# Kernel tuning notes

Measured on AMD Instinct MI355X. Metric: run time of the kernel, lower is better.

The kernel has to match this reference:

```python
import jax, jax.numpy as jnp
import numpy as np

NUM_HEADS = 16


def setup_inputs() -> dict:
    key = jax.random.key(0)
    ks = jax.random.split(key, 7)
    T, B, E = 2048, 2, 1024
    return {
        "query": jax.random.normal(ks[0], (T, B, E), jnp.float32),
        "key": jax.random.normal(ks[1], (T, B, E), jnp.float32),
        "value": jax.random.normal(ks[2], (T, B, E), jnp.float32),
        "query_pos": jax.random.normal(ks[3], (T, B, E), jnp.float32),
        "key_pos": jax.random.normal(ks[4], (T, B, E), jnp.float32),
        "W": jax.random.normal(ks[5], (E, E), jnp.float32) * (1.0 / np.sqrt(E)),
        "b": jax.random.normal(ks[6], (E,), jnp.float32) * 0.01,
    }


def reference(query, key, value, query_pos, key_pos, W, b):
    T, B, E = query.shape
    S = key.shape[0]
    H = NUM_HEADS
    D = E // H
    scale = jnp.asarray(D ** 0.5, query.dtype)

    identity = query  # residual uses query BEFORE positional add
    q = query + query_pos
    k = key + key_pos

    # (T,B,E) -> (B,H,T,D)
    q = q.reshape(T, B, H, D).transpose(1, 2, 0, 3)
    k = k.reshape(S, B, H, D).transpose(1, 2, 0, 3)
    v = value.reshape(S, B, H, D).transpose(1, 2, 0, 3)

    attn = jnp.einsum("bhtd,bhsd->bhts", q, k) / scale
    attn = jax.nn.softmax(attn, axis=-1)  # dropout p=0 -> identity

    out = jnp.einsum("bhts,bhsd->bhtd", attn, v)
    out = out.transpose(2, 0, 1, 3).reshape(T, B, E)  # (B,H,T,D)->(T,B,E)
    out = out @ W.T + b  # fuse_heads linear; out_dropout p=0 -> identity
    out = out + identity

    attn_avg = attn.sum(axis=1) / H  # average over heads -> (B,T,S)
    return out, attn_avg
```

## Files before the change

### kernel.cpp

```cpp
#include <hip/hip_runtime.h>
#include <hip/hip_bf16.h>

#define T_DIM 2048
#define S_DIM 2048
#define B_DIM 2
#define E_DIM 1024
#define H_DIM 16
#define D_DIM 64
#define EXP2S 0.18033688f
#define EXP2(x) __builtin_amdgcn_exp2f(x)

typedef unsigned short u16;
typedef unsigned int u32;
typedef float v4f __attribute__((ext_vector_type(4)));
typedef short v8s __attribute__((ext_vector_type(8)));
typedef short v4s __attribute__((ext_vector_type(4)));

__device__ __forceinline__ u16 f2bf(float f) {
    union { float f; u32 u; } x; x.f = f;
    return (u16)((x.u + 0x7fffu + ((x.u >> 16) & 1u)) >> 16);
}
__device__ __forceinline__ u32 pkrn(float lo, float hi) {
    union { __hip_bfloat162 h; u32 u; } c;
    c.h = __float22bfloat162_rn(make_float2(lo, hi));
    return c.u;
}
__device__ __forceinline__ v4f mfma16(v8s a, v8s b, v4f c) {
    return __builtin_amdgcn_mfma_f32_16x16x32_bf16(a, b, c, 0, 0, 0);
}
__device__ __forceinline__ v4f mfma16x16(v4s a, v4s b, v4f c) {
    return __builtin_amdgcn_mfma_f32_16x16x16bf16_1k(a, b, c, 0, 0, 0);
}
__device__ __forceinline__ v8s ld8(const u16* p) {
    return *reinterpret_cast<const v8s*>(p);
}

__global__ __launch_bounds__(256) void prep_qk(
    const float* __restrict__ q, const float* __restrict__ qp,
    const float* __restrict__ k, const float* __restrict__ kp,
    u16* __restrict__ qb, u16* __restrict__ ks) {
    int o = blockIdx.x * 256 + threadIdx.x;
    int d = o & 63, t = (o >> 6) & 2047, h = (o >> 17) & 15, b = o >> 21;
    int src = ((t * B_DIM + b) << 10) + (h << 6) + d;
    qb[o] = f2bf((q[src] + qp[src]) * EXP2S);
    ks[o] = f2bf(k[src] + kp[src]);
}

__global__ __launch_bounds__(256) void prep_w(const float* __restrict__ W, u16* __restrict__ Wb) {
    int o = blockIdx.x * 256 + threadIdx.x;
    Wb[o] = f2bf(W[o]);
}

__global__ __launch_bounds__(256) void prep_vt(const float* __restrict__ V, u16* __restrict__ vt) {
    __shared__ float tile[64 * 65];
    int bx = blockIdx.x;
    int bh = bx >> 5;
    int s0 = (bx & 31) * 64;
    int b = bh >> 4, h = bh & 15;
    int tid = threadIdx.x;
    int quarter = tid >> 6, c = tid & 63;
    int boff = b * E_DIM + h * 64;
#pragma unroll
    for (int p = 0; p < 16; ++p) {
        int r = quarter * 16 + p;
        tile[r * 65 + c] = V[(size_t)(s0 + r) * (B_DIM * E_DIM) + boff + c];
    }
    __syncthreads();
#pragma unroll
    for (int p = 0; p < 16; ++p) {
        int d = quarter * 16 + p;
        vt[(size_t)bh * (D_DIM * S_DIM) + (size_t)d * S_DIM + s0 + c] = f2bf(tile[c * 65 + d]);
    }
}

#define PITCH 72
__global__ __launch_bounds__(256) void attn_pv(
    const u16* __restrict__ qb, const u16* __restrict__ ks, const u16* __restrict__ vt,
    float* __restrict__ lin, u16* __restrict__ Xb) {
    __shared__ u16 Kl[2][64 * PITCH];
    __shared__ u16 Vl[2][64 * PITCH];

    int bx = blockIdx.x;
    int bh = bx >> 4;
    int b = bh >> 4, h = bh & 15;
    int tid = threadIdx.x;
    int w = tid >> 6;
    int tbase = (bx & 15) * 128 + w * 32;
    int lane = tid & 63;
    int m = lane & 15, g = lane >> 4;

    int srow = tid >> 2;
    int sqtr = (tid & 3) * 16;

    uint4 kr0, kr1, vr0, vr1;
    auto load_stage = [&](int s0) {
        const uint4* kp = reinterpret_cast<const uint4*>(
            ks + ((size_t)bh * S_DIM + s0 + srow) * 64 + sqtr);
        kr0 = kp[0]; kr1 = kp[1];
        const uint4* vp = reinterpret_cast<const uint4*>(
            vt + (size_t)bh * (D_DIM * S_DIM) + (size_t)srow * S_DIM + s0 + sqtr);
        vr0 = vp[0]; vr1 = vp[1];
    };
    auto write_stage = [&](int buf) {
        uint4* kd = reinterpret_cast<uint4*>(&Kl[buf][srow * PITCH + sqtr]);
        kd[0] = kr0; kd[1] = kr1;
        uint4* vd = reinterpret_cast<uint4*>(&Vl[buf][srow * PITCH + sqtr]);
        vd[0] = vr0; vd[1] = vr1;
    };

    const u16* qrow = qb + ((size_t)bh * T_DIM + tbase + m) * 64 + g * 8;
    v8s aq[2][2];
    aq[0][0] = ld8(qrow);        aq[0][1] = ld8(qrow + 32);
    aq[1][0] = ld8(qrow + 1024); aq[1][1] = ld8(qrow + 1024 + 32);

    v4f O[2][4];
    float lacc[2] = {0.f, 0.f};
#pragma unroll
    for (int tr = 0; tr < 2; ++tr)
#pragma unroll
        for (int dd = 0; dd < 4; ++dd) O[tr][dd] = (v4f){0.f, 0.f, 0.f, 0.f};

    load_stage(0);
    write_stage(0);
    load_stage(64);
    __syncthreads();

    for (int it = 0; it < 32; ++it) {
        int buf = it & 1;
        const u16* Kb = Kl[buf];
        const u16* Vb = Vl[buf];
#pragma unroll
        for (int ss = 0; ss < 4; ++ss) {
            v8s kf0 = ld8(&Kb[(ss * 16 + m) * PITCH + g * 8]);
            v8s kf1 = ld8(&Kb[(ss * 16 + m) * PITCH + 32 + g * 8]);
            v4s pa0, pa1;
            {
                v4f z = {0.f, 0.f, 0.f, 0.f};
                z = mfma16(kf0, aq[0][0], z);
                z = mfma16(kf1, aq[0][1], z);
                float e0 = EXP2(z[0]);
                float e1 = EXP2(z[1]);
                float e2 = EXP2(z[2]);
                float e3 = EXP2(z[3]);
                lacc[0] += (e0 + e1) + (e2 + e3);
                union { u32 u[2]; v4s s; } pk_;
                pk_.u[0] = pkrn(e0, e1);
                pk_.u[1] = pkrn(e2, e3);
                pa0 = pk_.s;
            }
            {
                v4f z = {0.f, 0.f, 0.f, 0.f};
                z = mfma16(kf0, aq[1][0], z);
                z = mfma16(kf1, aq[1][1], z);
                float e0 = EXP2(z[0]);
                float e1 = EXP2(z[1]);
                float e2 = EXP2(z[2]);
                float e3 = EXP2(z[3]);
                lacc[1] += (e0 + e1) + (e2 + e3);
                union { u32 u[2]; v4s s; } pk_;
                pk_.u[0] = pkrn(e0, e1);
                pk_.u[1] = pkrn(e2, e3);
                pa1 = pk_.s;
            }
#pragma unroll
            for (int dd = 0; dd < 4; ++dd) {
                v4s bv = *reinterpret_cast<const v4s*>(
                    &Vb[(dd * 16 + m) * PITCH + ss * 16 + g * 4]);
                O[0][dd] = mfma16x16(pa0, bv, O[0][dd]);
                O[1][dd] = mfma16x16(pa1, bv, O[1][dd]);
            }
        }
        if (it + 1 < 32) {
            write_stage(buf ^ 1);
            if (it + 2 < 32) load_stage((it + 2) * 64);
        }
        __syncthreads();
    }

#pragma unroll
    for (int tr = 0; tr < 2; ++tr) {
        lacc[tr] += __shfl_xor(lacc[tr], 16);
        lacc[tr] += __shfl_xor(lacc[tr], 32);
        float linv = 1.0f / lacc[tr];
        if (lane < 16) lin[(size_t)bh * T_DIM + tbase + tr * 16 + m] = linv;
#pragma unroll
        for (int r = 0; r < 4; ++r) {
            float lr = __shfl(linv, g * 4 + r);
            int t = tbase + tr * 16 + g * 4 + r;
#pragma unroll
            for (int dd = 0; dd < 4; ++dd)
                Xb[((size_t)t * B_DIM + b) * E_DIM + h * 64 + dd * 16 + m] =
                    f2bf(O[tr][dd][r] * lr);
        }
    }
}

__global__ __launch_bounds__(256, 4) void attn_avg(
    const u16* __restrict__ qb, const u16* __restrict__ ks,
    const float* __restrict__ lin, float* __restrict__ out1) {
    __shared__ u16 Kl[2][64 * PITCH];
    int bx = blockIdx.x;
    int b = bx >> 9;
    int tt = (bx >> 5) & 15;
    int st = bx & 31;
    int tid = threadIdx.x;
    int w = tid >> 6;
    int tbase = tt * 128 + w * 32;
    int sbase = st * 64;
    int lane = tid & 63, m = lane & 15, g = lane >> 4;

    int srow = tid >> 2;
    int sqtr = (tid & 3) * 16;

    uint4 kr0, kr1;
    auto load_stage = [&](int h) {
        const uint4* kp = reinterpret_cast<const uint4*>(
            ks + ((size_t)(b * 16 + h) * S_DIM + sbase + srow) * 64 + sqtr);
        kr0 = kp[0]; kr1 = kp[1];
    };
    auto write_stage = [&](int buf) {
        uint4* kd = reinterpret_cast<uint4*>(&Kl[buf][srow * PITCH + sqtr]);
        kd[0] = kr0; kd[1] = kr1;
    };

    v8s aqc00, aqc01, aqc10, aqc11, aqn00, aqn01, aqn10, aqn11;
    float livc[2][4], livn[2][4];
    auto load_q = [&](int h, v8s& a00, v8s& a01, v8s& a10, v8s& a11, float (&liv)[2][4]) {
        int bh = b * 16 + h;
        const u16* qrow = qb + ((size_t)bh * T_DIM + tbase + m) * 64 + g * 8;
        a00 = ld8(qrow);        a01 = ld8(qrow + 32);
        a10 = ld8(qrow + 1024); a11 = ld8(qrow + 1024 + 32);
#pragma unroll
        for (int tr = 0; tr < 2; ++tr)
#pragma unroll
            for (int r = 0; r < 4; ++r)
                liv[tr][r] = lin[(size_t)bh * T_DIM + tbase + tr * 16 + g * 4 + r] * (1.0f / 16.0f);
    };

    v4f AVG[2][4];
#pragma unroll
    for (int tr = 0; tr < 2; ++tr)
#pragma unroll
        for (int ss = 0; ss < 4; ++ss) AVG[tr][ss] = (v4f){0.f, 0.f, 0.f, 0.f};

    load_stage(0);
    write_stage(0);
    load_stage(1);
    load_q(0, aqc00, aqc01, aqc10, aqc11, livc);
    __syncthreads();

    for (int h = 0; h < H_DIM; ++h) {
        int buf = h & 1;
        if (h + 1 < H_DIM) load_q(h + 1, aqn00, aqn01, aqn10, aqn11, livn);

        const u16* Kb = Kl[buf];
#pragma unroll
        for (int ss = 0; ss < 4; ++ss) {
            v8s kf0 = ld8(&Kb[(ss * 16 + m) * PITCH + g * 8]);
            v8s kf1 = ld8(&Kb[(ss * 16 + m) * PITCH + 32 + g * 8]);
            {
                v4f z = {0.f, 0.f, 0.f, 0.f};
                z = mfma16(aqc00, kf0, z);
                z = mfma16(aqc01, kf1, z);
#pragma unroll
                for (int r = 0; r < 4; ++r)
                    AVG[0][ss][r] += EXP2(z[r]) * livc[0][r];
            }
            {
                v4f z = {0.f, 0.f, 0.f, 0.f};
                z = mfma16(aqc10, kf0, z);
                z = mfma16(aqc11, kf1, z);
#pragma unroll
                for (int r = 0; r < 4; ++r)
                    AVG[1][ss][r] += EXP2(z[r]) * livc[1][r];
            }
        }
        if (h + 1 < H_DIM) {
            write_stage(buf ^ 1);
            if (h + 2 < H_DIM) load_stage(h + 2);
        }
        __syncthreads();
        aqc00 = aqn00; aqc01 = aqn01; aqc10 = aqn10; aqc11 = aqn11;
#pragma unroll
        for (int tr = 0; tr < 2; ++tr)
#pragma unroll
            for (int r = 0; r < 4; ++r) livc[tr][r] = livn[tr][r];
    }
#pragma unroll
    for (int tr = 0; tr < 2; ++tr)
#pragma unroll
        for (int ss = 0; ss < 4; ++ss)
#pragma unroll
            for (int r = 0; r < 4; ++r) {
                int t = tbase + tr * 16 + g * 4 + r;
                out1[((size_t)b * T_DIM + t) * S_DIM + sbase + ss * 16 + m] = AVG[tr][ss][r];
            }
}

__global__ __launch_bounds__(256) void linear_mfma(
    const u16* __restrict__ Xb, const u16* __restrict__ Wb,
    const float* __restrict__ bias, const float* __restrict__ query,
    float* __restrict__ out0) {
    __shared__ u16 Al[2][64 * PITCH];
    __shared__ u16 Wl[2][128 * PITCH];
    int bx = blockIdx.x;
    int it = bx >> 3, jt = bx & 7;
    int tid = threadIdx.x;
    int w = tid >> 6;
    int lane = tid & 63;
    int m = lane & 15, g = lane >> 4;

    int arow = tid >> 2, aq4 = (tid & 3) * 16;
    int wrow = tid >> 1, wh2 = (tid & 1) * 32;

    uint4 ar0, ar1, wr0, wr1, wr2, wr3;
    auto load_stage = [&](int k0) {
        const uint4* ap = reinterpret_cast<const uint4*>(
            Xb + (size_t)(it * 64 + arow) * E_DIM + k0 + aq4);
        ar0 = ap[0]; ar1 = ap[1];
        const uint4* wp = reinterpret_cast<const uint4*>(
            Wb + (size_t)(jt * 128 + wrow) * E_DIM + k0 + wh2);
        wr0 = wp[0]; wr1 = wp[1]; wr2 = wp[2]; wr3 = wp[3];
    };
    auto write_stage = [&](int buf) {
        uint4* ad = reinterpret_cast<uint4*>(&Al[buf][arow * PITCH + aq4]);
        ad[0] = ar0; ad[1] = ar1;
        uint4* wd = reinterpret_cast<uint4*>(&Wl[buf][wrow * PITCH + wh2]);
        wd[0] = wr0; wd[1] = wr1; wd[2] = wr2; wd[3] = wr3;
    };

    v4f acc[4][2];
#pragma unroll
    for (int tr = 0; tr < 4; ++tr)
#pragma unroll
        for (int nn = 0; nn < 2; ++nn) acc[tr][nn] = (v4f){0.f, 0.f, 0.f, 0.f};

    load_stage(0);
    write_stage(0);
    load_stage(64);
    __syncthreads();

    for (int itk = 0; itk < 16; ++itk) {
        int buf = itk & 1;
        const u16* Ab = Al[buf];
        const u16* Ws = Wl[buf];
        v8s af[4][2], wf[2][2];
#pragma unroll
        for (int tr = 0; tr < 4; ++tr) {
            af[tr][0] = ld8(&Ab[(tr * 16 + m) * PITCH + g * 8]);
            af[tr][1] = ld8(&Ab[(tr * 16 + m) * PITCH + 32 + g * 8]);
        }
#pragma unroll
        for (int nn = 0; nn < 2; ++nn) {
            wf[nn][0] = ld8(&Ws[((w * 2 + nn) * 16 + m) * PITCH + g * 8]);
            wf[nn][1] = ld8(&Ws[((w * 2 + nn) * 16 + m) * PITCH + 32 + g * 8]);
        }
#pragma unroll
        for (int tr = 0; tr < 4; ++tr)
#pragma unroll
            for (int nn = 0; nn < 2; ++nn) {
                acc[tr][nn] = mfma16(af[tr][0], wf[nn][0], acc[tr][nn]);
                acc[tr][nn] = mfma16(af[tr][1], wf[nn][1], acc[tr][nn]);
            }
        if (itk + 1 < 16) {
            write_stage(buf ^ 1);
            if (itk + 2 < 16) load_stage((itk + 2) * 64);
        }
        __syncthreads();
    }

#pragma unroll
    for (int tr = 0; tr < 4; ++tr)
#pragma unroll
        for (int nn = 0; nn < 2; ++nn) {
            int col = jt * 128 + (w * 2 + nn) * 16 + m;
            float bv = bias[col];
#pragma unroll
            for (int r = 0; r < 4; ++r) {
                int row = it * 64 + tr * 16 + g * 4 + r;
                out0[(size_t)row * E_DIM + col] =
                    acc[tr][nn][r] + bv + query[(size_t)row * E_DIM + col];
            }
        }
}

extern "C" void kernel_launch(void* const* d_in, const int* in_sizes, int n_in,
                              void* d_out, int out_size, void* d_ws, size_t ws_size,
                              hipStream_t stream) {
    const float* query = (const float*)d_in[0];
    const float* key   = (const float*)d_in[1];
    const float* value = (const float*)d_in[2];
    const float* qpos  = (const float*)d_in[3];
    const float* kpos  = (const float*)d_in[4];
    const float* W     = (const float*)d_in[5];
    const float* bias  = (const float*)d_in[6];

    char* ws = (char*)d_ws;
    u16*   qb  = (u16*)(ws);
    u16*   ks  = (u16*)(ws + (size_t)( 8u << 20));
    u16*   vt  = (u16*)(ws + (size_t)(16u << 20));
    u16*   Wb  = (u16*)(ws + (size_t)(24u << 20));
    float* lin = (float*)(ws + (size_t)(26u << 20));
    u16*   Xb  = (u16*)(ws + (size_t)(27u << 20));

    float* out0 = (float*)d_out;
    float* out1 = out0 + (size_t)T_DIM * B_DIM * E_DIM;

    prep_qk<<<(B_DIM * H_DIM * T_DIM * D_DIM) / 256, 256, 0, stream>>>(query, qpos, key, kpos, qb, ks);
    prep_w<<<(E_DIM * E_DIM) / 256, 256, 0, stream>>>(W, Wb);
    prep_vt<<<B_DIM * H_DIM * (S_DIM / 64), 256, 0, stream>>>(value, vt);
    attn_pv<<<B_DIM * H_DIM * (T_DIM / 128), 256, 0, stream>>>(qb, ks, vt, lin, Xb);
    attn_avg<<<B_DIM * (T_DIM / 128) * (S_DIM / 64), 256, 0, stream>>>(qb, ks, lin, out1);
    linear_mfma<<<(T_DIM * B_DIM / 64) * (E_DIM / 128), 256, 0, stream>>>(Xb, Wb, bias, query, out0);
}
```

Baseline: 261.4 us.

## Split attention PV over two key halves with separate reduction kernel

The attention-PV kernel now splits the key/sequence dimension into two halves, doubling the grid from 512 to 1024 blocks so more of the GPU's compute units are busy. Each half writes unnormalized fp32 partial outputs and partial row sums into scratch space borrowed from the attn_avg output buffer. A new finalize kernel adds the partials, normalizes, converts to bf16 and writes the inverse sums. This trades extra global memory traffic and one more kernel launch for better occupancy. Correctness relies on attn_avg overwriting that borrowed region afterwards.

```diff
diff --git a/kernel.cpp b/kernel.cpp
--- a/kernel.cpp
+++ b/kernel.cpp
@@ -76,16 +76,19 @@
 #define PITCH 72
 __global__ __launch_bounds__(256) void attn_pv(
     const u16* __restrict__ qb, const u16* __restrict__ ks, const u16* __restrict__ vt,
-    float* __restrict__ lin, u16* __restrict__ Xb) {
+    float* __restrict__ O0, float* __restrict__ O1, float* __restrict__ lpart) {
     __shared__ u16 Kl[2][64 * PITCH];
     __shared__ u16 Vl[2][64 * PITCH];
 
     int bx = blockIdx.x;
-    int bh = bx >> 4;
+    int sh = bx & 1;
+    int tt = (bx >> 1) & 15;
+    int bh = bx >> 5;
     int b = bh >> 4, h = bh & 15;
     int tid = threadIdx.x;
     int w = tid >> 6;
-    int tbase = (bx & 15) * 128 + w * 32;
+    int tbase = tt * 128 + w * 32;
+    int sbase = sh * 1024;
     int lane = tid & 63;
     int m = lane & 15, g = lane >> 4;
 
@@ -120,12 +123,12 @@
 #pragma unroll
         for (int dd = 0; dd < 4; ++dd) O[tr][dd] = (v4f){0.f, 0.f, 0.f, 0.f};
 
-    load_stage(0);
+    load_stage(sbase);
     write_stage(0);
-    load_stage(64);
+    load_stage(sbase + 64);
     __syncthreads();
 
-    for (int it = 0; it < 32; ++it) {
+    for (int it = 0; it < 16; ++it) {
         int buf = it & 1;
         const u16* Kb = Kl[buf];
         const u16* Vb = Vl[buf];
@@ -170,29 +173,51 @@
                 O[1][dd] = mfma16x16(pa1, bv, O[1][dd]);
             }
         }
-        if (it + 1 < 32) {
+        if (it + 1 < 16) {
             write_stage(buf ^ 1);
-            if (it + 2 < 32) load_stage((it + 2) * 64);
+            if (it + 2 < 16) load_stage(sbase + (it + 2) * 64);
         }
         __syncthreads();
     }
 
+    float* Op = sh ? O1 : O0;
 #pragma unroll
     for (int tr = 0; tr < 2; ++tr) {
         lacc[tr] += __shfl_xor(lacc[tr], 16);
         lacc[tr] += __shfl_xor(lacc[tr], 32);
-        float linv = 1.0f / lacc[tr];
-        if (lane < 16) lin[(size_t)bh * T_DIM + tbase + tr * 16 + m] = linv;
+        if (lane < 16)
+            lpart[sh * (32 * T_DIM) + bh * T_DIM + tbase + tr * 16 + m] = lacc[tr];
 #pragma unroll
         for (int r = 0; r < 4; ++r) {
-            float lr = __shfl(linv, g * 4 + r);
             int t = tbase + tr * 16 + g * 4 + r;
 #pragma unroll
             for (int dd = 0; dd < 4; ++dd)
-                Xb[((size_t)t * B_DIM + b) * E_DIM + h * 64 + dd * 16 + m] =
-                    f2bf(O[tr][dd][r] * lr);
-        }
-    }
+                Op[((size_t)t * B_DIM + b) * E_DIM + h * 64 + dd * 16 + m] = O[tr][dd][r];
+        }
+    }
+}
+
+__global__ __launch_bounds__(256) void finalize_o(
+    const float* __restrict__ O0, const float* __restrict__ O1,
+    const float* __restrict__ lpart, u16* __restrict__ Xb, float* __restrict__ lin) {
+    int idx = blockIdx.x * 256 + threadIdx.x;
+    int i = idx * 4;
+    int t = i >> 11;
+    int be = i & 2047;
+    int b = be >> 10;
+    int e = be & 1023;
+    int bh = b * 16 + (e >> 6);
+    float l = lpart[bh * T_DIM + t] + lpart[32 * T_DIM + bh * T_DIM + t];
+    float linv = 1.0f / l;
+    float4 a = *reinterpret_cast<const float4*>(O0 + i);
+    float4 c = *reinterpret_cast<const float4*>(O1 + i);
+    ushort4 r4;
+    r4.x = f2bf((a.x + c.x) * linv);
+    r4.y = f2bf((a.y + c.y) * linv);
+    r4.z = f2bf((a.z + c.z) * linv);
+    r4.w = f2bf((a.w + c.w) * linv);
+    *reinterpret_cast<ushort4*>(Xb + i) = r4;
+    if ((e & 63) == 0) lin[bh * T_DIM + t] = linv;
 }
 
 __global__ __launch_bounds__(256, 4) void attn_avg(
@@ -402,14 +427,18 @@
     u16*   Wb  = (u16*)(ws + (size_t)(24u << 20));
     float* lin = (float*)(ws + (size_t)(26u << 20));
     u16*   Xb  = (u16*)(ws + (size_t)(27u << 20));
+    float* lpart = (float*)(ws + (size_t)(35u << 20));
 
     float* out0 = (float*)d_out;
     float* out1 = out0 + (size_t)T_DIM * B_DIM * E_DIM;
+    float* O0 = out1;
+    float* O1 = out1 + (size_t)T_DIM * B_DIM * E_DIM;
 
     prep_qk<<<(B_DIM * H_DIM * T_DIM * D_DIM) / 256, 256, 0, stream>>>(query, qpos, key, kpos, qb, ks);
     prep_w<<<(E_DIM * E_DIM) / 256, 256, 0, stream>>>(W, Wb);
     prep_vt<<<B_DIM * H_DIM * (S_DIM / 64), 256, 0, stream>>>(value, vt);
-    attn_pv<<<B_DIM * H_DIM * (T_DIM / 128), 256, 0, stream>>>(qb, ks, vt, lin, Xb);
+    attn_pv<<<B_DIM * H_DIM * (T_DIM / 128) * 2, 256, 0, stream>>>(qb, ks, vt, O0, O1, lpart);
+    finalize_o<<<(T_DIM * B_DIM * E_DIM / 4) / 256, 256, 0, stream>>>(O0, O1, lpart, Xb, lin);
     attn_avg<<<B_DIM * (T_DIM / 128) * (S_DIM / 64), 256, 0, stream>>>(qb, ks, lin, out1);
     linear_mfma<<<(T_DIM * B_DIM / 64) * (E_DIM / 128), 256, 0, stream>>>(Xb, Wb, bias, query, out0);
 }
```

After: 265.5 us. About the same (+1.6%).
